# Kernel tuning notes

Measured on AMD Instinct MI355X. Metric: run time of the kernel, lower is better.

## Reference

```python
import jax, jax.numpy as jnp
import numpy as np

NUM_HEADS = 16
ROPE_BASE = 10000.0
NEG_INF = float('-inf')


def _rotate_half_interleaved(x):
    # x: [..., d]; interleaved rotation: (-x2, x1) pairs
    x1 = x[..., ::2]
    x2 = x[..., 1::2]
    return jnp.stack((-x2, x1), axis=-1).reshape(x.shape)


def _rope_tables(seq_len, head_dim, dtype):
    inv_freq = 1.0 / (ROPE_BASE ** (jnp.arange(0, head_dim, 2, dtype=jnp.float32) / head_dim))
    pos = jnp.arange(seq_len, dtype=jnp.float32)
    freqs = pos[:, None] * inv_freq[None, :]          # [S, d/2]
    emb = jnp.concatenate((freqs, freqs), axis=-1)    # [S, d]  (HF-style concat, as in source)
    return jnp.cos(emb).astype(dtype), jnp.sin(emb).astype(dtype)


def setup_inputs() -> dict:
    key = jax.random.key(0)
    ks = jax.random.split(key, 4)
    B, S, H = 2, 2048, 2048
    scale = 0.02
    x = jax.random.normal(ks[0], (B, S, H), dtype=jnp.float32)
    qkv_w = jax.random.normal(ks[1], (3 * H, H), dtype=jnp.float32) * scale
    qkv_b = jnp.zeros((3 * H,), dtype=jnp.float32)
    out_w = jax.random.normal(ks[2], (H, H), dtype=jnp.float32) * scale
    out_b = jnp.zeros((H,), dtype=jnp.float32)
    attention_mask = jnp.ones((B, S), dtype=jnp.int32)
    return {"x": x, "attention_mask": attention_mask, "qkv_w": qkv_w,
            "qkv_b": qkv_b, "out_w": out_w, "out_b": out_b}


def reference(x, attention_mask, qkv_w, qkv_b, out_w, out_b):
    B, S, H = x.shape
    nh = NUM_HEADS
    hd = H // nh
    scale = hd ** -0.5

    qkv = x @ qkv_w.T + qkv_b                            # [B,S,3H]
    qkv = qkv.reshape(B, S, 3, nh, hd).transpose(2, 0, 3, 1, 4)  # [3,B,nh,S,hd]
    q, k, v = qkv[0], qkv[1], qkv[2]

    cos, sin = _rope_tables(S, hd, x.dtype)              # [S,hd]
    cos = cos[None, None, :, :]
    sin = sin[None, None, :, :]
    q = q * cos + _rotate_half_interleaved(q) * sin
    k = k * cos + _rotate_half_interleaved(k) * sin

    scores = jnp.einsum('bhqd,bhkd->bhqk', q, k) * scale  # [B,nh,S,S]
    causal = jnp.triu(jnp.ones((S, S), dtype=bool), k=1)
    scores = jnp.where(causal[None, None], NEG_INF, scores)
    key_mask = (attention_mask == 0)[:, None, None, :]    # [B,1,1,S]
    scores = jnp.where(key_mask, NEG_INF, scores)

    weights = jax.nn.softmax(scores, axis=-1)
    attn = jnp.einsum('bhqk,bhkd->bhqd', weights, v)       # [B,nh,S,hd]
    attn = attn.transpose(0, 2, 1, 3).reshape(B, S, H)
    return attn @ out_w.T + out_b
```

## Files before the change

kernel.cpp:

```cpp
#include <hip/hip_runtime.h>

typedef __bf16 bf16;
typedef __bf16 bf16x8 __attribute__((ext_vector_type(8)));
typedef float f32x4 __attribute__((ext_vector_type(4)));

#define MFMA_BF16(a, b, c) __builtin_amdgcn_mfma_f32_16x16x32_bf16(a, b, c, 0, 0, 0)

__device__ __forceinline__ void async16(const void* g, void* l) {
    __builtin_amdgcn_global_load_lds(
        (const __attribute__((address_space(1))) void*)g,
        (__attribute__((address_space(3))) void*)l,
        16, 0, 0);
}

__global__ void cvt8(const float* __restrict__ in, bf16* __restrict__ out, int n) {
    int i = (blockIdx.x * 256 + threadIdx.x) * 8;
    if (i >= n) return;
    float4 a = *(const float4*)(in + i);
    float4 b = *(const float4*)(in + i + 4);
    bf16x8 o;
    o[0] = (bf16)a.x; o[1] = (bf16)a.y; o[2] = (bf16)a.z; o[3] = (bf16)a.w;
    o[4] = (bf16)b.x; o[5] = (bf16)b.y; o[6] = (bf16)b.z; o[7] = (bf16)b.w;
    *(bf16x8*)(out + i) = o;
}

__global__ void tables_k(const int* __restrict__ am, float* __restrict__ cosT,
                         float* __restrict__ sinT, float* __restrict__ mbias) {
    int i = blockIdx.x * 256 + threadIdx.x;
    int s = i >> 7, d = i & 127, fi = d & 63;
    float inv = exp2f(-(float)fi * (13.287712379549449f / 64.0f));
    float ang = (float)s * inv;
    cosT[i] = cosf(ang);
    sinT[i] = sinf(ang);
    if (i < 2 * 2048) mbias[i] = (am[i] == 0) ? -1e30f : 0.0f;
}

template <int EPI>
__global__ void __launch_bounds__(256, 2)
gemm_bt(const bf16* __restrict__ A, const bf16* __restrict__ Bt,
        const float* __restrict__ bias, float* __restrict__ Cf,
        bf16* __restrict__ qb, bf16* __restrict__ kb, bf16* __restrict__ vtb,
        const float* __restrict__ cosT, const float* __restrict__ sinT,
        int M, int N, int K) {
    __shared__ __align__(16) bf16 sA[128 * 64];
    __shared__ __align__(16) bf16 sB[128 * 64];
    const int tid  = threadIdx.x;
    const int lane = tid & 63;
    const int quad = lane >> 4, l15 = lane & 15;
    const int wid = tid >> 6, wm = wid >> 1, wn = wid & 1;
    const int bm = blockIdx.x, bn = blockIdx.y;

    f32x4 acc[4][4];
#pragma unroll
    for (int i = 0; i < 4; i++)
#pragma unroll
        for (int j = 0; j < 4; j++)
#pragma unroll
            for (int c = 0; c < 4; c++) acc[i][j][c] = 0.0f;

    const int r0 = tid >> 3, x0 = tid & 7;
    const int g0 = x0 ^ (r0 & 7);
    const bf16* pa = A  + (size_t)(bm * 128 + r0) * K + g0 * 8;
    const bf16* pb = Bt + (size_t)(bn * 128 + r0) * K + g0 * 8;
    bf16* la = sA + tid * 8;
    bf16* lb = sB + tid * 8;
    const size_t gstep = (size_t)32 * K;

    for (int k0 = 0; k0 < K; k0 += 64) {
#pragma unroll
        for (int i = 0; i < 4; i++) {
            async16(pa + i * gstep, la + i * 2048);
            async16(pb + i * gstep, lb + i * 2048);
        }
        pa += 64; pb += 64;
        __syncthreads();
#pragma unroll
        for (int ks = 0; ks < 2; ks++) {
            bf16x8 af[4], bfr[4];
#pragma unroll
            for (int i = 0; i < 4; i++) {
                int r = wm * 64 + i * 16 + l15;
                int x = (ks * 4 + quad) ^ (r & 7);
                af[i] = *(const bf16x8*)(sA + r * 64 + x * 8);
            }
#pragma unroll
            for (int i = 0; i < 4; i++) {
                int r = wn * 64 + i * 16 + l15;
                int x = (ks * 4 + quad) ^ (r & 7);
                bfr[i] = *(const bf16x8*)(sB + r * 64 + x * 8);
            }
#pragma unroll
            for (int mi = 0; mi < 4; mi++)
#pragma unroll
                for (int ni = 0; ni < 4; ni++)
                    acc[mi][ni] = MFMA_BF16(af[mi], bfr[ni], acc[mi][ni]);
        }
        __syncthreads();
    }

    if (EPI == 0) {
#pragma unroll
        for (int mi = 0; mi < 4; mi++)
#pragma unroll
            for (int ni = 0; ni < 4; ni++) {
                int row0 = bm * 128 + wm * 64 + mi * 16 + quad * 4;
                int col  = bn * 128 + wn * 64 + ni * 16 + l15;
                float bv = bias[col];
#pragma unroll
                for (int r = 0; r < 4; r++)
                    Cf[(size_t)(row0 + r) * N + col] = acc[mi][ni][r] + bv;
            }
    } else {
#pragma unroll
        for (int mi = 0; mi < 4; mi++)
#pragma unroll
            for (int ni = 0; ni < 4; ni++) {
                int col   = bn * 128 + wn * 64 + ni * 16 + l15;
                int which = col >> 11;
                int hcol  = col & 2047;
                int h = hcol >> 7, d = hcol & 127;
                float bv = bias[col];
#pragma unroll
                for (int r = 0; r < 4; r++) {
                    int row = bm * 128 + wm * 64 + mi * 16 + quad * 4 + r;
                    int b = row >> 11, s = row & 2047;
                    float v  = acc[mi][ni][r] + bv;
                    float vp = __shfl_xor(v, 1, 64);
                    float ov = v;
                    if (which < 2) {
                        float c  = cosT[(s << 7) + d];
                        float sn = sinT[(s << 7) + d];
                        ov = v * c + ((d & 1) ? vp : -vp) * sn;
                    }
                    size_t bh = (size_t)(b * 16 + h);
                    if (which == 0)      qb[(bh * 2048 + s) * 128 + d] = (bf16)ov;
                    else if (which == 1) kb[(bh * 2048 + s) * 128 + d] = (bf16)ov;
                    else                 vtb[(bh * 128 + d) * 2048 + s] = (bf16)ov;
                }
            }
    }
}

__global__ void __launch_bounds__(256, 4)
fattn(const bf16* __restrict__ Q, const bf16* __restrict__ Kg,
      const bf16* __restrict__ Vt, const float* __restrict__ mbias,
      bf16* __restrict__ O) {
    __shared__ __align__(16) bf16 sK[64 * 128];
    __shared__ __align__(16) bf16 sV[128 * 64];
    __shared__ __align__(16) bf16 sP[4 * 16 * 64];
    const int tid = threadIdx.x, lane = tid & 63, w = tid >> 6;
    const int quad = lane >> 4, l15 = lane & 15;
    const int qt = 31 - (int)blockIdx.x;
    const int bh = blockIdx.y;
    const int b = bh >> 4, h = bh & 15;
    const int rowbase = qt * 64 + w * 16;

    const bf16* Qb  = Q  + (size_t)bh * 2048 * 128;
    const bf16* Kbh = Kg + (size_t)bh * 2048 * 128;
    const bf16* Vbh = Vt + (size_t)bh * 128 * 2048;
    const float* mbb = mbias + b * 2048;

    bf16x8 qf[4];
#pragma unroll
    for (int kq = 0; kq < 4; kq++)
        qf[kq] = *(const bf16x8*)(Qb + (size_t)(rowbase + l15) * 128 + kq * 32 + quad * 8);

    f32x4 oacc[8];
#pragma unroll
    for (int ni = 0; ni < 8; ni++)
#pragma unroll
        for (int c = 0; c < 4; c++) oacc[ni][c] = 0.0f;
    float m_s[4], l_s[4];
#pragma unroll
    for (int r = 0; r < 4; r++) { m_s[r] = -3e38f; l_s[r] = 0.0f; }

    const int rk = tid >> 4, xk = tid & 15, gk = xk ^ (rk & 15);
    const int rv = tid >> 3, xv = tid & 7,  gv = xv ^ (rv & 7);
    const int nkt = qt + 1;

    for (int kt = 0; kt < nkt; kt++) {
        const int kb0 = kt * 64;
#pragma unroll
        for (int i = 0; i < 4; i++) {
            async16(Kbh + (size_t)(kb0 + rk + i * 16) * 128 + gk * 8, sK + (i * 256 + tid) * 8);
            async16(Vbh + (size_t)(rv + i * 32) * 2048 + kb0 + gv * 8, sV + (i * 256 + tid) * 8);
        }
        __syncthreads();

        f32x4 sacc[4];
#pragma unroll
        for (int nj = 0; nj < 4; nj++)
#pragma unroll
            for (int c = 0; c < 4; c++) sacc[nj][c] = 0.0f;
#pragma unroll
        for (int kq = 0; kq < 4; kq++) {
            bf16x8 kf[4];
#pragma unroll
            for (int nj = 0; nj < 4; nj++) {
                int r = nj * 16 + l15;
                int x = (kq * 4 + quad) ^ (r & 15);
                kf[nj] = *(const bf16x8*)(sK + r * 128 + x * 8);
            }
#pragma unroll
            for (int nj = 0; nj < 4; nj++)
                sacc[nj] = MFMA_BF16(qf[kq], kf[nj], sacc[nj]);
        }

        float pv[4][4];
#pragma unroll
        for (int nj = 0; nj < 4; nj++) {
            int sk = kb0 + nj * 16 + l15;
            float mbv = mbb[sk];
#pragma unroll
            for (int r = 0; r < 4; r++) {
                int sq = rowbase + quad * 4 + r;
                float val = sacc[nj][r] * 0.08838834764831845f + mbv;
                pv[nj][r] = (sk > sq) ? -1e30f : val;
            }
        }

#pragma unroll
        for (int r = 0; r < 4; r++) {
            float mx = fmaxf(fmaxf(pv[0][r], pv[1][r]), fmaxf(pv[2][r], pv[3][r]));
#pragma unroll
            for (int off = 1; off <= 8; off <<= 1)
                mx = fmaxf(mx, __shfl_xor(mx, off, 64));
            float mnew  = fmaxf(m_s[r], mx);
            float alpha = __expf(m_s[r] - mnew);
            float rs = 0.0f;
#pragma unroll
            for (int nj = 0; nj < 4; nj++) {
                float p = __expf(pv[nj][r] - mnew);
                pv[nj][r] = p;
                rs += p;
            }
#pragma unroll
            for (int off = 1; off <= 8; off <<= 1)
                rs += __shfl_xor(rs, off, 64);
            l_s[r] = l_s[r] * alpha + rs;
            m_s[r] = mnew;
#pragma unroll
            for (int ni = 0; ni < 8; ni++) oacc[ni][r] *= alpha;
            int prow = quad * 4 + r;
#pragma unroll
            for (int nj = 0; nj < 4; nj++) {
                int col = nj * 16 + l15;
                int x = (col >> 3) ^ (prow & 7);
                sP[w * 1024 + prow * 64 + x * 8 + (col & 7)] = (bf16)pv[nj][r];
            }
        }

#pragma unroll
        for (int kq2 = 0; kq2 < 2; kq2++) {
            int rp = l15;
            int xp = (kq2 * 4 + quad) ^ (rp & 7);
            bf16x8 pf = *(const bf16x8*)(sP + w * 1024 + rp * 64 + xp * 8);
#pragma unroll
            for (int ni = 0; ni < 8; ni++) {
                int r = ni * 16 + l15;
                int x = (kq2 * 4 + quad) ^ (r & 7);
                bf16x8 vf = *(const bf16x8*)(sV + r * 64 + x * 8);
                oacc[ni] = MFMA_BF16(pf, vf, oacc[ni]);
            }
        }
        __syncthreads();
    }

#pragma unroll
    for (int r = 0; r < 4; r++) {
        int s = rowbase + quad * 4 + r;
        float inv = 1.0f / l_s[r];
        size_t base = ((size_t)(b * 2048 + s)) * 2048 + h * 128;
#pragma unroll
        for (int ni = 0; ni < 8; ni++)
            O[base + ni * 16 + l15] = (bf16)(oacc[ni][r] * inv);
    }
}

extern "C" void kernel_launch(void* const* d_in, const int* in_sizes, int n_in,
                              void* d_out, int out_size, void* d_ws, size_t ws_size,
                              hipStream_t stream) {
    const float* x     = (const float*)d_in[0];
    const int*   am    = (const int*)d_in[1];
    const float* qkvw  = (const float*)d_in[2];
    const float* qkvb  = (const float*)d_in[3];
    const float* outw  = (const float*)d_in[4];
    const float* outb  = (const float*)d_in[5];
    float* out = (float*)d_out;

    char* ws = (char*)d_ws;
    bf16*  xb    = (bf16*)(ws);
    bf16*  wqkv  = (bf16*)(ws + (16ull << 20));
    bf16*  wout  = (bf16*)(ws + (40ull << 20));
    bf16*  qb    = (bf16*)(ws + (48ull << 20));
    bf16*  kb    = (bf16*)(ws + (64ull << 20));
    bf16*  vtb   = (bf16*)(ws + (80ull << 20));
    bf16*  attn  = (bf16*)(ws + (96ull << 20));
    float* cosT  = (float*)(ws + (112ull << 20));
    float* sinT  = (float*)(ws + (113ull << 20));
    float* mbias = (float*)(ws + (114ull << 20));

    cvt8<<<4096, 256, 0, stream>>>(x, xb, 4096 * 2048);
    cvt8<<<6144, 256, 0, stream>>>(qkvw, wqkv, 6144 * 2048);
    cvt8<<<2048, 256, 0, stream>>>(outw, wout, 2048 * 2048);
    tables_k<<<1024, 256, 0, stream>>>(am, cosT, sinT, mbias);

    gemm_bt<1><<<dim3(32, 48), 256, 0, stream>>>(
        xb, wqkv, qkvb, nullptr, qb, kb, vtb, cosT, sinT, 4096, 6144, 2048);

    fattn<<<dim3(32, 32), 256, 0, stream>>>(qb, kb, vtb, mbias, attn);

    gemm_bt<0><<<dim3(32, 16), 256, 0, stream>>>(
        attn, wout, outb, out, nullptr, nullptr, nullptr, nullptr, nullptr,
        4096, 2048, 2048);
}
```

Measured before the change: 451.1 us.

## Transpose MFMA operands so each lane owns one query row in flash attention

Swaps the MFMA operand order for QK^T and PV so the accumulator is transposed. Each lane now holds a single query row across its four registers, which replaces per-register softmax state and 4-step row shuffles with a scalar running max/sum and two cross-quad shuffles. The mask bias is loaded as float4, P is written to LDS in 4-element runs, and the output is stored as bf16x4 vectors. The softmax scale is also folded into Q in the projection epilogue, dropping a multiply per score at the cost of rounding the scaled Q to bf16.

```diff
diff --git a/kernel.cpp b/kernel.cpp
--- a/kernel.cpp
+++ b/kernel.cpp
@@ -1,6 +1,7 @@
 #include <hip/hip_runtime.h>
 
 typedef __bf16 bf16;
+typedef __bf16 bf16x4 __attribute__((ext_vector_type(4)));
 typedef __bf16 bf16x8 __attribute__((ext_vector_type(8)));
 typedef float f32x4 __attribute__((ext_vector_type(4)));
 
@@ -132,6 +133,7 @@
                         float sn = sinT[(s << 7) + d];
                         ov = v * c + ((d & 1) ? vp : -vp) * sn;
                     }
+                    if (which == 0) ov *= 0.08838834764831845f;
                     size_t bh = (size_t)(b * 16 + h);
                     if (which == 0)      qb[(bh * 2048 + s) * 128 + d] = (bf16)ov;
                     else if (which == 1) kb[(bh * 2048 + s) * 128 + d] = (bf16)ov;
@@ -154,6 +156,7 @@
     const int bh = blockIdx.y;
     const int b = bh >> 4, h = bh & 15;
     const int rowbase = qt * 64 + w * 16;
+    const int myq = rowbase + l15;
 
     const bf16* Qb  = Q  + (size_t)bh * 2048 * 128;
     const bf16* Kbh = Kg + (size_t)bh * 2048 * 128;
@@ -163,16 +166,14 @@
     bf16x8 qf[4];
 #pragma unroll
     for (int kq = 0; kq < 4; kq++)
-        qf[kq] = *(const bf16x8*)(Qb + (size_t)(rowbase + l15) * 128 + kq * 32 + quad * 8);
+        qf[kq] = *(const bf16x8*)(Qb + (size_t)myq * 128 + kq * 32 + quad * 8);
 
     f32x4 oacc[8];
 #pragma unroll
     for (int ni = 0; ni < 8; ni++)
 #pragma unroll
         for (int c = 0; c < 4; c++) oacc[ni][c] = 0.0f;
-    float m_s[4], l_s[4];
-#pragma unroll
-    for (int r = 0; r < 4; r++) { m_s[r] = -3e38f; l_s[r] = 0.0f; }
+    float m_s = -3e38f, l_s = 0.0f;
 
     const int rk = tid >> 4, xk = tid & 15, gk = xk ^ (rk & 15);
     const int rv = tid >> 3, xv = tid & 7,  gv = xv ^ (rv & 7);
@@ -203,77 +204,78 @@
             }
 #pragma unroll
             for (int nj = 0; nj < 4; nj++)
-                sacc[nj] = MFMA_BF16(qf[kq], kf[nj], sacc[nj]);
+                sacc[nj] = MFMA_BF16(kf[nj], qf[kq], sacc[nj]);
         }
 
         float pv[4][4];
 #pragma unroll
         for (int nj = 0; nj < 4; nj++) {
-            int sk = kb0 + nj * 16 + l15;
-            float mbv = mbb[sk];
+            float4 mb4 = *(const float4*)(mbb + kb0 + nj * 16 + quad * 4);
 #pragma unroll
             for (int r = 0; r < 4; r++) {
-                int sq = rowbase + quad * 4 + r;
-                float val = sacc[nj][r] * 0.08838834764831845f + mbv;
-                pv[nj][r] = (sk > sq) ? -1e30f : val;
-            }
-        }
-
-#pragma unroll
-        for (int r = 0; r < 4; r++) {
-            float mx = fmaxf(fmaxf(pv[0][r], pv[1][r]), fmaxf(pv[2][r], pv[3][r]));
-#pragma unroll
-            for (int off = 1; off <= 8; off <<= 1)
-                mx = fmaxf(mx, __shfl_xor(mx, off, 64));
-            float mnew  = fmaxf(m_s[r], mx);
-            float alpha = __expf(m_s[r] - mnew);
-            float rs = 0.0f;
-#pragma unroll
-            for (int nj = 0; nj < 4; nj++) {
+                int sk = kb0 + nj * 16 + quad * 4 + r;
+                float val = sacc[nj][r] + ((const float*)&mb4)[r];
+                pv[nj][r] = (sk > myq) ? -1e30f : val;
+            }
+        }
+
+        float mx = -3e38f;
+#pragma unroll
+        for (int nj = 0; nj < 4; nj++)
+#pragma unroll
+            for (int r = 0; r < 4; r++) mx = fmaxf(mx, pv[nj][r]);
+        mx = fmaxf(mx, __shfl_xor(mx, 16, 64));
+        mx = fmaxf(mx, __shfl_xor(mx, 32, 64));
+        float mnew  = fmaxf(m_s, mx);
+        float alpha = __expf(m_s - mnew);
+        float rs = 0.0f;
+#pragma unroll
+        for (int nj = 0; nj < 4; nj++)
+#pragma unroll
+            for (int r = 0; r < 4; r++) {
                 float p = __expf(pv[nj][r] - mnew);
                 pv[nj][r] = p;
                 rs += p;
             }
-#pragma unroll
-            for (int off = 1; off <= 8; off <<= 1)
-                rs += __shfl_xor(rs, off, 64);
-            l_s[r] = l_s[r] * alpha + rs;
-            m_s[r] = mnew;
-#pragma unroll
-            for (int ni = 0; ni < 8; ni++) oacc[ni][r] *= alpha;
-            int prow = quad * 4 + r;
-#pragma unroll
-            for (int nj = 0; nj < 4; nj++) {
-                int col = nj * 16 + l15;
-                int x = (col >> 3) ^ (prow & 7);
-                sP[w * 1024 + prow * 64 + x * 8 + (col & 7)] = (bf16)pv[nj][r];
-            }
+        rs += __shfl_xor(rs, 16, 64);
+        rs += __shfl_xor(rs, 32, 64);
+        l_s = l_s * alpha + rs;
+        m_s = mnew;
+#pragma unroll
+        for (int ni = 0; ni < 8; ni++) oacc[ni] *= alpha;
+
+#pragma unroll
+        for (int nj = 0; nj < 4; nj++) {
+            int chunk = nj * 2 + (quad >> 1);
+            int x = chunk ^ (l15 & 7);
+            bf16* dst = sP + w * 1024 + l15 * 64 + x * 8 + (quad & 1) * 4;
+#pragma unroll
+            for (int r = 0; r < 4; r++) dst[r] = (bf16)pv[nj][r];
         }
 
 #pragma unroll
         for (int kq2 = 0; kq2 < 2; kq2++) {
-            int rp = l15;
-            int xp = (kq2 * 4 + quad) ^ (rp & 7);
-            bf16x8 pf = *(const bf16x8*)(sP + w * 1024 + rp * 64 + xp * 8);
+            int xp = (kq2 * 4 + quad) ^ (l15 & 7);
+            bf16x8 pf = *(const bf16x8*)(sP + w * 1024 + l15 * 64 + xp * 8);
 #pragma unroll
             for (int ni = 0; ni < 8; ni++) {
                 int r = ni * 16 + l15;
                 int x = (kq2 * 4 + quad) ^ (r & 7);
                 bf16x8 vf = *(const bf16x8*)(sV + r * 64 + x * 8);
-                oacc[ni] = MFMA_BF16(pf, vf, oacc[ni]);
+                oacc[ni] = MFMA_BF16(vf, pf, oacc[ni]);
             }
         }
         __syncthreads();
     }
 
-#pragma unroll
-    for (int r = 0; r < 4; r++) {
-        int s = rowbase + quad * 4 + r;
-        float inv = 1.0f / l_s[r];
-        size_t base = ((size_t)(b * 2048 + s)) * 2048 + h * 128;
-#pragma unroll
-        for (int ni = 0; ni < 8; ni++)
-            O[base + ni * 16 + l15] = (bf16)(oacc[ni][r] * inv);
+    float inv = 1.0f / l_s;
+    size_t base = ((size_t)(b * 2048 + myq)) * 2048 + h * 128;
+#pragma unroll
+    for (int ni = 0; ni < 8; ni++) {
+        bf16x4 o4;
+#pragma unroll
+        for (int r = 0; r < 4; r++) o4[r] = (bf16)(oacc[ni][r] * inv);
+        *(bf16x4*)(O + base + ni * 16 + quad * 4) = o4;
     }
 }
 
```

After: 429.5 us. 1.05x faster.
